# Optimization experiments

Hardware: AMD Instinct MI355X
Metric: run time of the kernel (lower is better)

## Reference

```python
import jax, jax.numpy as jnp
import numpy as np

N = 262144   # total atoms (rows of x)
B = 512      # systems (segments)
E = 16       # experts
I = 256      # in_features
O_MOE = 128  # moe out channels (fraction_moe=0.5 of 256)
O_REG = 128  # regular Linear out channels


def setup_inputs() -> dict:
    key = jax.random.key(0)
    ks = jax.random.split(key, 6)
    k = 1.0 / np.sqrt(I)
    x = jax.random.normal(ks[0], (N, I), dtype=jnp.float32)
    coeff = jax.random.uniform(ks[1], (B, E), dtype=jnp.float32)
    routing_idxs = jnp.full((B,), N // B, dtype=jnp.int64)  # uniform segment lengths
    moe_weights = k * 2.0 * (jax.random.uniform(ks[2], (E, O_MOE, I), dtype=jnp.float32) - 0.5)
    moe_bias = k * 2.0 * (jax.random.uniform(ks[3], (O_MOE,), dtype=jnp.float32) - 0.5)
    lin_weight = k * 2.0 * (jax.random.uniform(ks[4], (O_REG, I), dtype=jnp.float32) - 0.5)
    lin_bias = k * 2.0 * (jax.random.uniform(ks[5], (O_REG,), dtype=jnp.float32) - 0.5)
    return {"x": x, "expert_mixing_coefficients": coeff, "routing_idxs": routing_idxs,
            "moe_weights": moe_weights, "moe_bias": moe_bias,
            "lin_weight": lin_weight, "lin_bias": lin_bias}


def reference(x, expert_mixing_coefficients, routing_idxs, moe_weights, moe_bias, lin_weight, lin_bias):
    b = expert_mixing_coefficients.shape[0]
    n, i = x.shape
    l = n // b  # uniform segment length (segment_mm with equal routing_idxs)
    # per-system mixed expert weights: [B, I, O_moe]
    w_mixed = jnp.einsum('eoi,be->bio', moe_weights, expert_mixing_coefficients)
    # grouped segment matmul: rows of segment b multiply w_mixed[b]
    moe_out = jnp.einsum('bli,bio->blo', x.reshape(b, l, i), w_mixed).reshape(n, -1) + moe_bias
    regular_out = x @ lin_weight.T + lin_bias
    return jnp.concatenate([moe_out, regular_out], axis=-1)
```

## Files before the change

### kernel.cpp

```cpp
#include <hip/hip_runtime.h>


#define NATOMS 262144
#define NSEG   512
#define NEXP   16
#define KDIM   256
#define OMOE   128
#define OTOT   256
#define LSEG   512
#define BM     128
#define BK     32

typedef __attribute__((ext_vector_type(4))) float  f32x4;
typedef __attribute__((ext_vector_type(8))) short  bf16x8;
typedef __attribute__((ext_vector_type(4))) unsigned short u16x4;

__device__ __forceinline__ unsigned short bf16_rne(float v) {
  unsigned u = __builtin_bit_cast(unsigned, v);
  unsigned r = u + 0x7FFFu + ((u >> 16) & 1u);
  return (unsigned short)(r >> 16);
}

__device__ __forceinline__ void split2(float v, unsigned short& h, unsigned short& l) {
  h = bf16_rne(v);
  float hf = __builtin_bit_cast(float, ((unsigned)h) << 16);
  l = bf16_rne(v - hf);
}

__global__ __launch_bounds__(256) void prep_moe_kernel(
    const float* __restrict__ moe_w, const float* __restrict__ coeff,
    unsigned short* __restrict__ wm_hi, unsigned short* __restrict__ wm_lo) {
  __shared__ float wlds[NEXP][4][KDIM];
  const int t  = threadIdx.x;
  const int ot = blockIdx.x & 31;
  const int bc = blockIdx.x >> 5;
  const float* src = moe_w + (size_t)ot * 4 * KDIM;
  #pragma unroll
  for (int it = 0; it < 16; ++it) {
    int idx = it * 256 + t;
    int e = idx >> 8;
    int rem = idx & 255;
    int o = rem >> 6, k4 = rem & 63;
    *(f32x4*)(&wlds[e][o][k4 * 4]) =
        *(const f32x4*)(src + (size_t)e * OMOE * KDIM + o * KDIM + k4 * 4);
  }
  __syncthreads();
  const int o = t >> 6, k4 = t & 63;
  const int og = ot * 4 + o;
  for (int bb = 0; bb < 32; ++bb) {
    const int b = bc * 32 + bb;
    const float* cf = coeff + (size_t)b * NEXP;
    f32x4 acc = (f32x4){0.f, 0.f, 0.f, 0.f};
    #pragma unroll
    for (int e = 0; e < NEXP; ++e) {
      const float c = cf[e];
      const f32x4 w = *(const f32x4*)(&wlds[e][o][k4 * 4]);
      #pragma unroll
      for (int j = 0; j < 4; ++j) acc[j] += c * w[j];
    }
    u16x4 hv, lv;
    #pragma unroll
    for (int j = 0; j < 4; ++j) {
      unsigned short h, l;
      split2(acc[j], h, l);
      hv[j] = h; lv[j] = l;
    }
    const size_t base = ((size_t)b * OMOE + og) * KDIM + k4 * 4;
    *(u16x4*)(wm_hi + base) = hv;
    *(u16x4*)(wm_lo + base) = lv;
  }
}

__global__ __launch_bounds__(256) void prep_lin_kernel(
    const float* __restrict__ lw,
    unsigned short* __restrict__ wl_hi, unsigned short* __restrict__ wl_lo) {
  const int idx = blockIdx.x * 256 + threadIdx.x;
  f32x4 v = *(const f32x4*)(lw + (size_t)idx * 4);
  u16x4 hv, lv;
  #pragma unroll
  for (int j = 0; j < 4; ++j) {
    unsigned short h, l;
    split2(v[j], h, l);
    hv[j] = h; lv[j] = l;
  }
  *(u16x4*)(wl_hi + (size_t)idx * 4) = hv;
  *(u16x4*)(wl_lo + (size_t)idx * 4) = lv;
}

#define GLOAD16(g, l) __builtin_amdgcn_global_load_lds(                      \
    (const __attribute__((address_space(1))) unsigned int*)(g),              \
    (__attribute__((address_space(3))) unsigned int*)(l), 16, 0, 0)

__global__ __launch_bounds__(512, 1) void gemm_kernel(
    const float* __restrict__ x,
    const unsigned short* __restrict__ wm_hi, const unsigned short* __restrict__ wm_lo,
    const unsigned short* __restrict__ wl_hi, const unsigned short* __restrict__ wl_lo,
    const float* __restrict__ moe_b, const float* __restrict__ lin_b,
    float* __restrict__ out) {
  __shared__ unsigned short lds[49152];
  const int t = threadIdx.x;
  const int wave = t >> 6, lane = t & 63;
  const int wm = wave >> 1, wn = wave & 1;

  const int blk = blockIdx.x;
  const int wg = ((blk & 7) << 8) | (blk >> 3);
  const int b = wg >> 2, rt = wg & 3;
  const int row0 = b * LSEG + rt * BM;

  f32x4 acc[2][8];
  #pragma unroll
  for (int mt = 0; mt < 2; ++mt)
    #pragma unroll
    for (int nt = 0; nt < 8; ++nt) acc[mt][nt] = (f32x4){0.f, 0.f, 0.f, 0.f};

  const int arow = t >> 2, aks = t & 3;
  const int aoff = (wm * 32 + (lane & 15)) * 32 + (lane >> 4) * 8;
  const int boff = (wn * 128 + (lane & 15)) * 32 + (lane >> 4) * 8;

  auto stage_B = [&](int buf, int kt) {
    unsigned short* Bb = &lds[16384 + buf * 16384];
    #pragma unroll
    for (int part = 0; part < 2; ++part) {
      const unsigned short* gm = part ? wm_lo : wm_hi;
      const unsigned short* gl = part ? wl_lo : wl_hi;
      #pragma unroll
      for (int cc = 0; cc < 2; ++cc) {
        const int c = wave * 2 + cc;
        const int o = c * 16 + (lane >> 2);
        const int ks = lane & 3;
        const unsigned short* src = (c < 8)
            ? (gm + ((size_t)b * OMOE + o) * KDIM + kt * BK + ks * 8)
            : (gl + (size_t)(o - OMOE) * KDIM + kt * BK + ks * 8);
        GLOAD16(src, Bb + part * 8192 + c * 512);
      }
    }
  };

  auto write_A = [&](int buf, f32x4 v0, f32x4 v1) {
    bf16x8 hv, lv;
    #pragma unroll
    for (int j = 0; j < 4; ++j) {
      unsigned short h, l;
      split2(v0[j], h, l); hv[j] = (short)h;     lv[j] = (short)l;
      split2(v1[j], h, l); hv[4 + j] = (short)h; lv[4 + j] = (short)l;
    }
    unsigned short* Ab = &lds[buf * 8192 + arow * 32 + aks * 8];
    *(bf16x8*)(Ab) = hv;
    *(bf16x8*)(Ab + 4096) = lv;
  };

  auto compute = [&](int buf) {
    const short* Ab = (const short*)&lds[buf * 8192];
    const short* Bb = (const short*)&lds[16384 + buf * 16384];
    bf16x8 ah[2], al[2];
    #pragma unroll
    for (int mt = 0; mt < 2; ++mt) {
      ah[mt] = *(const bf16x8*)(Ab + aoff + mt * 512);
      al[mt] = *(const bf16x8*)(Ab + 4096 + aoff + mt * 512);
    }
    #pragma unroll
    for (int nt = 0; nt < 8; ++nt) {
      bf16x8 bh = *(const bf16x8*)(Bb + boff + nt * 512);
      bf16x8 bl = *(const bf16x8*)(Bb + 8192 + boff + nt * 512);
      #pragma unroll
      for (int mt = 0; mt < 2; ++mt) {
        acc[mt][nt] = __builtin_amdgcn_mfma_f32_16x16x32_bf16(ah[mt], bh, acc[mt][nt], 0, 0, 0);
        acc[mt][nt] = __builtin_amdgcn_mfma_f32_16x16x32_bf16(ah[mt], bl, acc[mt][nt], 0, 0, 0);
        acc[mt][nt] = __builtin_amdgcn_mfma_f32_16x16x32_bf16(al[mt], bh, acc[mt][nt], 0, 0, 0);
      }
    }
  };

  stage_B(0, 0);
  {
    const float* xp = x + (size_t)(row0 + arow) * KDIM + aks * 8;
    write_A(0, *(const f32x4*)xp, *(const f32x4*)(xp + 4));
  }
  __syncthreads();

  int buf = 0;
  for (int kt = 0; kt < 8; ++kt) {
    f32x4 v0, v1;
    const bool pf = (kt < 7);
    if (pf) {
      const float* xp = x + (size_t)(row0 + arow) * KDIM + (kt + 1) * BK + aks * 8;
      v0 = *(const f32x4*)xp;
      v1 = *(const f32x4*)(xp + 4);
      stage_B(buf ^ 1, kt + 1);
    }
    compute(buf);
    if (pf) write_A(buf ^ 1, v0, v1);
    __syncthreads();
    buf ^= 1;
  }

  #pragma unroll
  for (int nt = 0; nt < 8; ++nt) {
    const int col = wn * 128 + nt * 16 + (lane & 15);
    const float bias = (col < OMOE) ? moe_b[col] : lin_b[col - OMOE];
    #pragma unroll
    for (int mt = 0; mt < 2; ++mt) {
      const int rbase = row0 + wm * 32 + mt * 16 + (lane >> 4) * 4;
      #pragma unroll
      for (int j = 0; j < 4; ++j)
        out[(size_t)(rbase + j) * OTOT + col] = acc[mt][nt][j] + bias;
    }
  }
}

extern "C" void kernel_launch(void* const* d_in, const int* in_sizes, int n_in,
                              void* d_out, int out_size, void* d_ws, size_t ws_size,
                              hipStream_t stream) {
  const float* x     = (const float*)d_in[0];
  const float* coeff = (const float*)d_in[1];
  const float* moe_w = (const float*)d_in[3];
  const float* moe_b = (const float*)d_in[4];
  const float* lin_w = (const float*)d_in[5];
  const float* lin_b = (const float*)d_in[6];
  float* out = (float*)d_out;

  unsigned short* wm_hi = (unsigned short*)d_ws;
  unsigned short* wm_lo = wm_hi + (size_t)NSEG * OMOE * KDIM;
  unsigned short* wl_hi = wm_lo + (size_t)NSEG * OMOE * KDIM;
  unsigned short* wl_lo = wl_hi + (size_t)OMOE * KDIM;

  prep_moe_kernel<<<dim3(512), dim3(256), 0, stream>>>(moe_w, coeff, wm_hi, wm_lo);
  prep_lin_kernel<<<dim3(32), dim3(256), 0, stream>>>(lin_w, wl_hi, wl_lo);
  gemm_kernel<<<dim3(2048), dim3(512), 0, stream>>>(x, wm_hi, wm_lo, wl_hi, wl_lo,
                                                    moe_b, lin_b, out);
}
```

Before: 520.9 us.

## Load A fragments directly to registers and pre-swizzle B tiles for contiguous LDS staging

The GEMM now loads x straight from global memory into MFMA A-fragment registers and splits it to bf16 hi/lo with packed v_cvt_pk_bf16_f32 conversions, so the A tile no longer passes through LDS. The prep kernels write weights in a k-tile-major, XOR-swizzled, hi/lo-interleaved layout, so each B stage is a contiguous copy and the LDS fragment reads avoid bank conflicts. LDS use drops to 64KB and launch bounds now allow several blocks per CU. The cost is less coalesced x loads (each lane reads 32B at a row stride) and more register pressure from holding the fragments; the hardware RNE conversion may also round slightly differently from the software version.

```diff
diff --git a/kernel.cpp b/kernel.cpp
--- a/kernel.cpp
+++ b/kernel.cpp
@@ -1,35 +1,54 @@
 #include <hip/hip_runtime.h>
 
 
-#define NATOMS 262144
 #define NSEG   512
 #define NEXP   16
 #define KDIM   256
 #define OMOE   128
 #define OTOT   256
 #define LSEG   512
-#define BM     128
-#define BK     32
 
 typedef __attribute__((ext_vector_type(4))) float  f32x4;
 typedef __attribute__((ext_vector_type(8))) short  bf16x8;
 typedef __attribute__((ext_vector_type(4))) unsigned short u16x4;
+typedef __attribute__((ext_vector_type(4))) unsigned int   u32x4;
 
 __device__ __forceinline__ unsigned short bf16_rne(float v) {
   unsigned u = __builtin_bit_cast(unsigned, v);
   unsigned r = u + 0x7FFFu + ((u >> 16) & 1u);
   return (unsigned short)(r >> 16);
 }
-
 __device__ __forceinline__ void split2(float v, unsigned short& h, unsigned short& l) {
   h = bf16_rne(v);
   float hf = __builtin_bit_cast(float, ((unsigned)h) << 16);
   l = bf16_rne(v - hf);
 }
+__device__ __forceinline__ unsigned cvtpk(float a, float b) {
+  unsigned r;
+  asm("v_cvt_pk_bf16_f32 %0, %1, %2" : "=v"(r) : "v"(a), "v"(b));
+  return r;
+}
+__device__ __forceinline__ void split8(f32x4 v0, f32x4 v1, bf16x8& h, bf16x8& l) {
+  float a[8] = {v0[0], v0[1], v0[2], v0[3], v1[0], v1[1], v1[2], v1[3]};
+  unsigned hw[4], lw[4];
+  #pragma unroll
+  for (int i = 0; i < 4; ++i) {
+    unsigned hp = cvtpk(a[2 * i], a[2 * i + 1]);
+    float hf0 = __builtin_bit_cast(float, hp << 16);
+    float hf1 = __builtin_bit_cast(float, hp & 0xFFFF0000u);
+    lw[i] = cvtpk(a[2 * i] - hf0, a[2 * i + 1] - hf1);
+    hw[i] = hp;
+  }
+  u32x4 H = {hw[0], hw[1], hw[2], hw[3]};
+  u32x4 L = {lw[0], lw[1], lw[2], lw[3]};
+  h = __builtin_bit_cast(bf16x8, H);
+  l = __builtin_bit_cast(bf16x8, L);
+}
+
 
 __global__ __launch_bounds__(256) void prep_moe_kernel(
     const float* __restrict__ moe_w, const float* __restrict__ coeff,
-    unsigned short* __restrict__ wm_hi, unsigned short* __restrict__ wm_lo) {
+    unsigned short* __restrict__ wm) {
   __shared__ float wlds[NEXP][4][KDIM];
   const int t  = threadIdx.x;
   const int ot = blockIdx.x & 31;
@@ -38,8 +57,7 @@
   #pragma unroll
   for (int it = 0; it < 16; ++it) {
     int idx = it * 256 + t;
-    int e = idx >> 8;
-    int rem = idx & 255;
+    int e = idx >> 8, rem = idx & 255;
     int o = rem >> 6, k4 = rem & 63;
     *(f32x4*)(&wlds[e][o][k4 * 4]) =
         *(const f32x4*)(src + (size_t)e * OMOE * KDIM + o * KDIM + k4 * 4);
@@ -47,6 +65,9 @@
   __syncthreads();
   const int o = t >> 6, k4 = t & 63;
   const int og = ot * 4 + o;
+  const int kt = k4 >> 3, ks = (k4 >> 1) & 3, jo = (k4 & 1) * 4;
+  const int p  = og * 4 + (ks ^ ((og >> 1) & 3));
+  const size_t woff = (size_t)kt * 8192 + p * 8 + jo;
   for (int bb = 0; bb < 32; ++bb) {
     const int b = bc * 32 + bb;
     const float* cf = coeff + (size_t)b * NEXP;
@@ -65,17 +86,19 @@
       split2(acc[j], h, l);
       hv[j] = h; lv[j] = l;
     }
-    const size_t base = ((size_t)b * OMOE + og) * KDIM + k4 * 4;
-    *(u16x4*)(wm_hi + base) = hv;
-    *(u16x4*)(wm_lo + base) = lv;
+    unsigned short* dst = wm + (size_t)b * 65536 + woff;
+    *(u16x4*)(dst)        = hv;
+    *(u16x4*)(dst + 4096) = lv;
   }
 }
 
 __global__ __launch_bounds__(256) void prep_lin_kernel(
-    const float* __restrict__ lw,
-    unsigned short* __restrict__ wl_hi, unsigned short* __restrict__ wl_lo) {
+    const float* __restrict__ lw, unsigned short* __restrict__ wl) {
   const int idx = blockIdx.x * 256 + threadIdx.x;
+  const int o = idx >> 6, k4 = idx & 63;
   f32x4 v = *(const f32x4*)(lw + (size_t)idx * 4);
+  const int kt = k4 >> 3, ks = (k4 >> 1) & 3, jo = (k4 & 1) * 4;
+  const int p  = o * 4 + (ks ^ ((o >> 1) & 3));
   u16x4 hv, lv;
   #pragma unroll
   for (int j = 0; j < 4; ++j) {
@@ -83,85 +106,65 @@
     split2(v[j], h, l);
     hv[j] = h; lv[j] = l;
   }
-  *(u16x4*)(wl_hi + (size_t)idx * 4) = hv;
-  *(u16x4*)(wl_lo + (size_t)idx * 4) = lv;
+  unsigned short* dst = wl + (size_t)kt * 8192 + p * 8 + jo;
+  *(u16x4*)(dst)        = hv;
+  *(u16x4*)(dst + 4096) = lv;
 }
 
 #define GLOAD16(g, l) __builtin_amdgcn_global_load_lds(                      \
     (const __attribute__((address_space(1))) unsigned int*)(g),              \
     (__attribute__((address_space(3))) unsigned int*)(l), 16, 0, 0)
 
-__global__ __launch_bounds__(512, 1) void gemm_kernel(
+__global__ __launch_bounds__(512, 4) void gemm_kernel(
     const float* __restrict__ x,
-    const unsigned short* __restrict__ wm_hi, const unsigned short* __restrict__ wm_lo,
-    const unsigned short* __restrict__ wl_hi, const unsigned short* __restrict__ wl_lo,
+    const unsigned short* __restrict__ wm, const unsigned short* __restrict__ wl,
     const float* __restrict__ moe_b, const float* __restrict__ lin_b,
     float* __restrict__ out) {
-  __shared__ unsigned short lds[49152];
+  __shared__ unsigned short lds[32768];
   const int t = threadIdx.x;
   const int wave = t >> 6, lane = t & 63;
-  const int wm = wave >> 1, wn = wave & 1;
+  const int wrm = wave >> 1, wn = wave & 1;
 
   const int blk = blockIdx.x;
   const int wg = ((blk & 7) << 8) | (blk >> 3);
   const int b = wg >> 2, rt = wg & 3;
-  const int row0 = b * LSEG + rt * BM;
-
-  f32x4 acc[2][8];
-  #pragma unroll
-  for (int mt = 0; mt < 2; ++mt)
-    #pragma unroll
-    for (int nt = 0; nt < 8; ++nt) acc[mt][nt] = (f32x4){0.f, 0.f, 0.f, 0.f};
-
-  const int arow = t >> 2, aks = t & 3;
-  const int aoff = (wm * 32 + (lane & 15)) * 32 + (lane >> 4) * 8;
-  const int boff = (wn * 128 + (lane & 15)) * 32 + (lane >> 4) * 8;
+  const int row0 = b * LSEG + rt * 128;
+
+  f32x4 acc[2][8] = {};
+
+  const float* xbase = x + (size_t)(row0 + wrm * 32 + (lane & 15)) * KDIM + (lane >> 4) * 8;
+
+  const int colb = wn * 128 + (lane & 15);
+  const int ks = lane >> 4;
+  const int boff0 = (colb * 4 + (ks ^ ((colb >> 1) & 3))) * 8;
+
+  const unsigned short* wmb = wm + (size_t)b * 65536;
 
   auto stage_B = [&](int buf, int kt) {
-    unsigned short* Bb = &lds[16384 + buf * 16384];
+    unsigned short* Bb = &lds[buf * 16384];
+    const unsigned short* srcm = wmb + (size_t)kt * 8192;
+    const unsigned short* srcl = wl  + (size_t)kt * 8192;
     #pragma unroll
     for (int part = 0; part < 2; ++part) {
-      const unsigned short* gm = part ? wm_lo : wm_hi;
-      const unsigned short* gl = part ? wl_lo : wl_hi;
       #pragma unroll
       for (int cc = 0; cc < 2; ++cc) {
         const int c = wave * 2 + cc;
-        const int o = c * 16 + (lane >> 2);
-        const int ks = lane & 3;
         const unsigned short* src = (c < 8)
-            ? (gm + ((size_t)b * OMOE + o) * KDIM + kt * BK + ks * 8)
-            : (gl + (size_t)(o - OMOE) * KDIM + kt * BK + ks * 8);
+            ? (srcm + (size_t)part * 4096 + (c * 64 + lane) * 8)
+            : (srcl + (size_t)part * 4096 + ((c - 8) * 64 + lane) * 8);
         GLOAD16(src, Bb + part * 8192 + c * 512);
       }
     }
   };
 
-  auto write_A = [&](int buf, f32x4 v0, f32x4 v1) {
-    bf16x8 hv, lv;
-    #pragma unroll
-    for (int j = 0; j < 4; ++j) {
-      unsigned short h, l;
-      split2(v0[j], h, l); hv[j] = (short)h;     lv[j] = (short)l;
-      split2(v1[j], h, l); hv[4 + j] = (short)h; lv[4 + j] = (short)l;
-    }
-    unsigned short* Ab = &lds[buf * 8192 + arow * 32 + aks * 8];
-    *(bf16x8*)(Ab) = hv;
-    *(bf16x8*)(Ab + 4096) = lv;
-  };
+  bf16x8 ah[2], al[2];
 
   auto compute = [&](int buf) {
-    const short* Ab = (const short*)&lds[buf * 8192];
-    const short* Bb = (const short*)&lds[16384 + buf * 16384];
-    bf16x8 ah[2], al[2];
-    #pragma unroll
-    for (int mt = 0; mt < 2; ++mt) {
-      ah[mt] = *(const bf16x8*)(Ab + aoff + mt * 512);
-      al[mt] = *(const bf16x8*)(Ab + 4096 + aoff + mt * 512);
-    }
+    const short* Bb = (const short*)&lds[buf * 16384];
     #pragma unroll
     for (int nt = 0; nt < 8; ++nt) {
-      bf16x8 bh = *(const bf16x8*)(Bb + boff + nt * 512);
-      bf16x8 bl = *(const bf16x8*)(Bb + 8192 + boff + nt * 512);
+      bf16x8 bh = *(const bf16x8*)(Bb + boff0 + nt * 512);
+      bf16x8 bl = *(const bf16x8*)(Bb + 8192 + boff0 + nt * 512);
       #pragma unroll
       for (int mt = 0; mt < 2; ++mt) {
         acc[mt][nt] = __builtin_amdgcn_mfma_f32_16x16x32_bf16(ah[mt], bh, acc[mt][nt], 0, 0, 0);
@@ -173,23 +176,29 @@
 
   stage_B(0, 0);
   {
-    const float* xp = x + (size_t)(row0 + arow) * KDIM + aks * 8;
-    write_A(0, *(const f32x4*)xp, *(const f32x4*)(xp + 4));
+    const float* p0 = xbase;
+    const float* p1 = xbase + 16 * KDIM;
+    split8(*(const f32x4*)p0, *(const f32x4*)(p0 + 4), ah[0], al[0]);
+    split8(*(const f32x4*)p1, *(const f32x4*)(p1 + 4), ah[1], al[1]);
   }
   __syncthreads();
 
   int buf = 0;
   for (int kt = 0; kt < 8; ++kt) {
-    f32x4 v0, v1;
     const bool pf = (kt < 7);
+    f32x4 n0, n1, n2, n3;
     if (pf) {
-      const float* xp = x + (size_t)(row0 + arow) * KDIM + (kt + 1) * BK + aks * 8;
-      v0 = *(const f32x4*)xp;
-      v1 = *(const f32x4*)(xp + 4);
+      const float* p0 = xbase + (kt + 1) * 32;
+      const float* p1 = p0 + 16 * KDIM;
+      n0 = *(const f32x4*)p0; n1 = *(const f32x4*)(p0 + 4);
+      n2 = *(const f32x4*)p1; n3 = *(const f32x4*)(p1 + 4);
       stage_B(buf ^ 1, kt + 1);
     }
     compute(buf);
-    if (pf) write_A(buf ^ 1, v0, v1);
+    if (pf) {
+      split8(n0, n1, ah[0], al[0]);
+      split8(n2, n3, ah[1], al[1]);
+    }
     __syncthreads();
     buf ^= 1;
   }
@@ -200,7 +209,7 @@
     const float bias = (col < OMOE) ? moe_b[col] : lin_b[col - OMOE];
     #pragma unroll
     for (int mt = 0; mt < 2; ++mt) {
-      const int rbase = row0 + wm * 32 + mt * 16 + (lane >> 4) * 4;
+      const int rbase = row0 + wrm * 32 + mt * 16 + (lane >> 4) * 4;
       #pragma unroll
       for (int j = 0; j < 4; ++j)
         out[(size_t)(rbase + j) * OTOT + col] = acc[mt][nt][j] + bias;
@@ -219,13 +228,10 @@
   const float* lin_b = (const float*)d_in[6];
   float* out = (float*)d_out;
 
-  unsigned short* wm_hi = (unsigned short*)d_ws;
-  unsigned short* wm_lo = wm_hi + (size_t)NSEG * OMOE * KDIM;
-  unsigned short* wl_hi = wm_lo + (size_t)NSEG * OMOE * KDIM;
-  unsigned short* wl_lo = wl_hi + (size_t)OMOE * KDIM;
-
-  prep_moe_kernel<<<dim3(512), dim3(256), 0, stream>>>(moe_w, coeff, wm_hi, wm_lo);
-  prep_lin_kernel<<<dim3(32), dim3(256), 0, stream>>>(lin_w, wl_hi, wl_lo);
-  gemm_kernel<<<dim3(2048), dim3(512), 0, stream>>>(x, wm_hi, wm_lo, wl_hi, wl_lo,
-                                                    moe_b, lin_b, out);
-}
+  unsigned short* wm = (unsigned short*)d_ws;
+  unsigned short* wl = wm + (size_t)NSEG * 65536;
+
+  prep_moe_kernel<<<dim3(512), dim3(256), 0, stream>>>(moe_w, coeff, wm);
+  prep_lin_kernel<<<dim3(32), dim3(256), 0, stream>>>(lin_w, wl);
+  gemm_kernel<<<dim3(2048), dim3(512), 0, stream>>>(x, wm, wl, moe_b, lin_b, out);
+}
```

Result: no change. 517.0 us (-0.8%).
